# Kernel optimization log

Measured on AMD Instinct MI355X. Metric: run time of the kernel, lower is better.

Reference implementation:

```python
import jax, jax.numpy as jnp
import numpy as np

N = 100000
E = 3200000
NEG_SLOPE = 0.2


def _gat(x, W, a_src, a_dst, b, src, dst, n):
    """PyG-style GATConv (eval mode, self-loops already appended to src/dst)."""
    H, C = a_src.shape
    h = (x @ W).reshape(n, H, C)                       # [N,H,C]
    es = jnp.einsum('nhc,hc->nh', h, a_src)            # per-node src logits
    ed = jnp.einsum('nhc,hc->nh', h, a_dst)
    e = jax.nn.leaky_relu(es[src] + ed[dst], NEG_SLOPE)  # [E,H]
    m = jax.ops.segment_max(e, dst, num_segments=n)    # stable softmax per dst
    ee = jnp.exp(e - m[dst])
    z = jax.ops.segment_sum(ee, dst, num_segments=n)
    alpha = ee / z[dst]                                # softmax over in-edges
    out = jax.ops.segment_sum(h[src] * alpha[:, :, None], dst, num_segments=n)
    return out.reshape(n, H * C) + b


def setup_inputs() -> dict:
    key = jax.random.key(0)
    ks = jax.random.split(key, 25)
    rn = lambda k, s, sc=0.1: jax.random.normal(k, s, dtype=jnp.float32) * sc
    return {
        'x1': rn(ks[0], (N, 8), 1.0),
        'x2': rn(ks[1], (N, 10), 1.0),
        'edge_index': jax.random.randint(ks[2], (2, E), 0, N, dtype=jnp.int32),
        'num_nodes': N,
        'Wq': rn(ks[3], (8, 16)), 'bq': rn(ks[4], (16,)),
        'Wk': rn(ks[5], (10, 16)), 'bk': rn(ks[6], (16,)),
        'Wv': rn(ks[7], (18, 16)), 'bv': rn(ks[8], (16,)),
        'W1': rn(ks[9], (16, 32)), 'a1s': rn(ks[10], (8, 4)), 'a1d': rn(ks[11], (8, 4)), 'b1': rn(ks[12], (32,)),
        'W2': rn(ks[13], (32, 16)), 'a2s': rn(ks[14], (4, 4)), 'a2d': rn(ks[15], (4, 4)), 'b2': rn(ks[16], (16,)),
        'W3': rn(ks[17], (16, 8)), 'a3s': rn(ks[18], (2, 4)), 'a3d': rn(ks[19], (2, 4)), 'b3': rn(ks[20], (8,)),
        'Wl2': rn(ks[21], (8, 1)),
    }


def reference(x1, x2, edge_index, num_nodes, Wq, bq, Wk, bk, Wv, bv,
              W1, a1s, a1d, b1, W2, a2s, a2d, b2, W3, a3s, a3d, b3, Wl2):
    n = num_nodes
    q = x1 @ Wq + bq                                   # [N,16]
    k = x2 @ Wk + bk                                   # [N,16]
    v = jnp.concatenate([x1, x2], axis=1) @ Wv + bv    # [N,16]
    score = jnp.sum(q * k, axis=1)                     # bmm(q[:,None,:], k[:,:,None]).squeeze()
    attw = jax.nn.softmax(score)[:, None]              # softmax over all nodes
    fused = attw * v                                   # [N,16]

    sl = jnp.arange(n, dtype=edge_index.dtype)         # GATConv adds self-loops
    src = jnp.concatenate([edge_index[0], sl])
    dst = jnp.concatenate([edge_index[1], sl])

    h1 = _gat(fused, W1, a1s, a1d, b1, src, dst, n)    # [N,32]
    h2 = _gat(h1, W2, a2s, a2d, b2, src, dst, n)       # [N,16]
    x4 = _gat(h2, W3, a3s, a3d, b3, src, dst, n)       # [N,8]; dropout=identity (eval)

    # Row-normalized adjacency (no self loops), expressed as O(E) segment ops.
    r, c = edge_index[0], edge_index[1]
    deg = jax.ops.segment_sum(jnp.ones_like(r, dtype=x4.dtype), r, num_segments=n)
    inv = jnp.where(deg > 0, 1.0 / deg, 0.0)[:, None]
    R3 = jax.ops.segment_sum(x4[c], r, num_segments=n) * inv  # Adj_norm @ x4
    local = jnp.sum(x4 * R3, axis=1, keepdims=True)    # sum_j Adjn[i,j]*(x4_i . x4_j)
    glob = R3 @ Wl2                                    # lin2 (no bias)
    return local + glob                                # [N,1]
```

## Files before the change

kernel.cpp:

```cpp
#include <hip/hip_runtime.h>

#define TPB 256
#define NBMAX 1024
#define CAP 9216
#define EPB 2048

typedef float f32x4 __attribute__((ext_vector_type(4)));
typedef float f32x2 __attribute__((ext_vector_type(2)));

__device__ __forceinline__ float lrelu(float x) { return x > 0.f ? x : 0.2f * x; }

__device__ __forceinline__ unsigned bfr(float x) {
  unsigned u = __float_as_uint(x);
  return (u + 0x7FFFu + ((u >> 16) & 1u)) >> 16;
}
__device__ __forceinline__ unsigned pk(float a, float b) { return bfr(a) | (bfr(b) << 16); }
__device__ __forceinline__ float ubf(unsigned us) { return __uint_as_float(us << 16); }

__global__ void __launch_bounds__(TPB) k_bucket(
    const int* __restrict__ ei, int E, int N,
    int* __restrict__ cursor, unsigned* __restrict__ items)
{
  __shared__ int hist[NBMAX];
  __shared__ int lofs[NBMAX];
  __shared__ int basem[NBMAX];
  __shared__ int scan_s[TPB];
  __shared__ unsigned stage[2 * EPB];
  __shared__ unsigned short bid[2 * EPB];
  int tid = threadIdx.x;
  for (int i = tid; i < NBMAX; i += TPB) hist[i] = 0;
  int s0 = blockIdx.x * EPB;
  int nE = min(EPB, E - s0);
  int sv[EPB / TPB], dv[EPB / TPB];
  __syncthreads();
#pragma unroll
  for (int k = 0; k < EPB / (TPB * 4); k++) {
    int li = tid * 4 + k * TPB * 4;
    if (li + 3 < nE) {
      int4 s4 = *(const int4*)(ei + s0 + li);
      int4 d4 = *(const int4*)(ei + E + s0 + li);
      sv[k*4+0] = s4.x; sv[k*4+1] = s4.y; sv[k*4+2] = s4.z; sv[k*4+3] = s4.w;
      dv[k*4+0] = d4.x; dv[k*4+1] = d4.y; dv[k*4+2] = d4.z; dv[k*4+3] = d4.w;
#pragma unroll
      for (int j = 0; j < 4; j++) {
        atomicAdd(&hist[dv[k*4+j] >> 8], 1);
        atomicAdd(&hist[(N + sv[k*4+j]) >> 8], 1);
      }
    } else {
      for (int j = 0; j < 4; j++) {
        if (li + j < nE) {
          sv[k*4+j] = ei[s0 + li + j];
          dv[k*4+j] = ei[E + s0 + li + j];
          atomicAdd(&hist[dv[k*4+j] >> 8], 1);
          atomicAdd(&hist[(N + sv[k*4+j]) >> 8], 1);
        }
      }
    }
  }
  __syncthreads();
  int b0 = tid * 4;
  int c0 = hist[b0], c1 = hist[b0 + 1], c2 = hist[b0 + 2], c3 = hist[b0 + 3];
  int tsum = c0 + c1 + c2 + c3;
  scan_s[tid] = tsum;
  __syncthreads();
#pragma unroll
  for (int o = 1; o < TPB; o <<= 1) {
    int t = (tid >= o) ? scan_s[tid - o] : 0;
    __syncthreads();
    scan_s[tid] += t;
    __syncthreads();
  }
  int run = scan_s[tid] - tsum;
  int cs[4] = {c0, c1, c2, c3};
#pragma unroll
  for (int j = 0; j < 4; j++) {
    int b = b0 + j, c = cs[j];
    lofs[b] = run;
    int resv = c ? atomicAdd(&cursor[b], c) : 0;
    basem[b] = b * CAP + resv - run;
    hist[b] = 0;
    run += c;
  }
  __syncthreads();
#pragma unroll
  for (int k = 0; k < EPB / TPB; k++) {
    int li = tid * 4 + (k >> 2) * TPB * 4 + (k & 3);
    if (li < nE) {
      int s = sv[k], d = dv[k];
      int b1 = d >> 8;
      int p1 = lofs[b1] + atomicAdd(&hist[b1], 1);
      stage[p1] = ((unsigned)(d & 255) << 24) | (unsigned)s;
      bid[p1] = (unsigned short)b1;
      int k2 = N + s, b2 = k2 >> 8;
      int p2 = lofs[b2] + atomicAdd(&hist[b2], 1);
      stage[p2] = ((unsigned)(k2 & 255) << 24) | (unsigned)d;
      bid[p2] = (unsigned short)b2;
    }
  }
  __syncthreads();
  int total = 2 * nE;
  for (int idx = tid; idx < total; idx += TPB) {
    unsigned u = stage[idx];
    int b = bid[idx];
    int dest = basem[b] + idx;
    if (dest < (b + 1) * CAP) items[dest] = u;
  }
}

__global__ void __launch_bounds__(TPB) k_csr(
    const int* __restrict__ cursor, unsigned* __restrict__ items,
    int* __restrict__ rowptr, int* __restrict__ rowend, int n2)
{
  __shared__ unsigned stage[CAP];
  __shared__ int cnt_s[TPB], scan_s[TPB], off_s[TPB];
  int tid = threadIdx.x, b = blockIdx.x;
  size_t bbase = (size_t)b * CAP;
  int cnt = min(cursor[b], CAP);
  int c4 = cnt & ~3;
  for (int i = tid * 4; i < c4; i += TPB * 4) {
    uint4 v = *(const uint4*)(items + bbase + i);
    stage[i] = v.x; stage[i+1] = v.y; stage[i+2] = v.z; stage[i+3] = v.w;
  }
  for (int i = c4 + tid; i < cnt; i += TPB) stage[i] = items[bbase + i];
  cnt_s[tid] = 0;
  __syncthreads();
  for (int i = tid; i < cnt; i += TPB) atomicAdd(&cnt_s[stage[i] >> 24], 1);
  __syncthreads();
  int v = cnt_s[tid];
  scan_s[tid] = v;
  __syncthreads();
#pragma unroll
  for (int o = 1; o < TPB; o <<= 1) {
    int t = (tid >= o) ? scan_s[tid - o] : 0;
    __syncthreads();
    scan_s[tid] += t;
    __syncthreads();
  }
  int excl = scan_s[tid] - v;
  off_s[tid] = excl;
  int g = b * 256 + tid;
  if (g < n2) { rowptr[g] = (int)bbase + excl; rowend[g] = (int)bbase + excl + v; }
  cnt_s[tid] = 0;
  __syncthreads();
  for (int i = tid; i < cnt; i += TPB) {
    unsigned u = stage[i];
    int k = u >> 24;
    int r = atomicAdd(&cnt_s[k], 1);
    items[bbase + off_s[k] + r] = u & 0xFFFFFFu;
  }
}


__global__ void __launch_bounds__(TPB) k_score(
    const float* __restrict__ x1, const float* __restrict__ x2,
    const float* __restrict__ Wq, const float* __restrict__ bq,
    const float* __restrict__ Wk, const float* __restrict__ bk,
    float* __restrict__ escore, float* __restrict__ sumexp, int N)
{
  __shared__ float sWq[128], sWk[160], sbq[16], sbk[16];
  for (int i = threadIdx.x; i < 128; i += TPB) sWq[i] = Wq[i];
  for (int i = threadIdx.x; i < 160; i += TPB) sWk[i] = Wk[i];
  if (threadIdx.x < 16) { sbq[threadIdx.x] = bq[threadIdx.x]; sbk[threadIdx.x] = bk[threadIdx.x]; }
  __syncthreads();
  int n = blockIdx.x * TPB + threadIdx.x;
  float e = 0.f;
  if (n < N) {
    float a[8], b[10];
#pragma unroll
    for (int i = 0; i < 8; i++) a[i] = x1[n*8 + i];
#pragma unroll
    for (int i = 0; i < 10; i++) b[i] = x2[n*10 + i];
    float score = 0.f;
#pragma unroll
    for (int j = 0; j < 16; j++) {
      float q = sbq[j], k = sbk[j];
#pragma unroll
      for (int i = 0; i < 8; i++) q += a[i] * sWq[i*16 + j];
#pragma unroll
      for (int i = 0; i < 10; i++) k += b[i] * sWk[i*16 + j];
      score += q * k;
    }
    e = __expf(score);
    escore[n] = e;
  }
  float v = e;
#pragma unroll
  for (int off = 32; off > 0; off >>= 1) v += __shfl_down(v, off);
  __shared__ float red[TPB / 64];
  if ((threadIdx.x & 63) == 0) red[threadIdx.x >> 6] = v;
  __syncthreads();
  if (threadIdx.x == 0) {
    float s = 0.f;
#pragma unroll
    for (int w = 0; w < TPB / 64; w++) s += red[w];
    atomicAdd(sumexp, s);
  }
}

__global__ void __launch_bounds__(TPB) k_A1(
    const float* __restrict__ x1, const float* __restrict__ x2,
    const float* __restrict__ Wv, const float* __restrict__ bv,
    const float* __restrict__ W1, const float* __restrict__ a1s, const float* __restrict__ a1d,
    const float* __restrict__ escore, const float* __restrict__ sumexp,
    unsigned* __restrict__ rec1a, unsigned* __restrict__ rec1b,
    float* __restrict__ ed, int N)
{
  __shared__ float sWv[288], sbv[16], sW1[512], sas[32], sad[32];
  for (int i = threadIdx.x; i < 288; i += TPB) sWv[i] = Wv[i];
  for (int i = threadIdx.x; i < 512; i += TPB) sW1[i] = W1[i];
  if (threadIdx.x < 16) sbv[threadIdx.x] = bv[threadIdx.x];
  if (threadIdx.x < 32) { sas[threadIdx.x] = a1s[threadIdx.x]; sad[threadIdx.x] = a1d[threadIdx.x]; }
  __syncthreads();
  int n = blockIdx.x * TPB + threadIdx.x;
  if (n >= N) return;
  float w = escore[n] / sumexp[0];
  float f[16];
  {
    float a[8], b[10];
#pragma unroll
    for (int i = 0; i < 8; i++) a[i] = x1[n*8 + i];
#pragma unroll
    for (int i = 0; i < 10; i++) b[i] = x2[n*10 + i];
#pragma unroll
    for (int j = 0; j < 16; j++) {
      float v = sbv[j];
#pragma unroll
      for (int i = 0; i < 8; i++) v += a[i] * sWv[i*16 + j];
#pragma unroll
      for (int i = 0; i < 10; i++) v += b[i] * sWv[(8 + i)*16 + j];
      f[j] = w * v;
    }
  }
  float hr[32], esv[8], edv[8];
#pragma unroll
  for (int j = 0; j < 32; j++) {
    float s = 0.f;
#pragma unroll
    for (int i = 0; i < 16; i++) s += f[i] * sW1[i*32 + j];
    hr[j] = s;
  }
#pragma unroll
  for (int hh = 0; hh < 8; hh++) {
    float s = 0.f, d = 0.f;
#pragma unroll
    for (int c = 0; c < 4; c++) { s += hr[hh*4+c]*sas[hh*4+c]; d += hr[hh*4+c]*sad[hh*4+c]; }
    esv[hh] = s; edv[hh] = d;
  }
  unsigned* ra = rec1a + (size_t)n*10;
  unsigned* rb = rec1b + (size_t)n*10;
  ra[0] = pk(esv[0], esv[1]); ra[1] = pk(esv[2], esv[3]);
  rb[0] = pk(esv[4], esv[5]); rb[1] = pk(esv[6], esv[7]);
#pragma unroll
  for (int hh = 0; hh < 4; hh++) {
    ra[2+2*hh] = pk(hr[hh*4+0], hr[hh*4+1]);
    ra[3+2*hh] = pk(hr[hh*4+2], hr[hh*4+3]);
    rb[2+2*hh] = pk(hr[16+hh*4+0], hr[16+hh*4+1]);
    rb[3+2*hh] = pk(hr[16+hh*4+2], hr[16+hh*4+3]);
  }
  f32x4 e0 = {edv[0], edv[1], edv[2], edv[3]};
  f32x4 e1 = {edv[4], edv[5], edv[6], edv[7]};
  *(f32x4*)(ed + n*8)     = e0;
  *(f32x4*)(ed + n*8 + 4) = e1;
}

__global__ void __launch_bounds__(TPB) k_B2(
    const float* __restrict__ W2, const float* __restrict__ a2s, const float* __restrict__ a2d,
    const float* __restrict__ X,
    unsigned* __restrict__ rec2, float* __restrict__ ed, int N)
{
  __shared__ float sW[512], sas[16], sad[16];
  for (int i = threadIdx.x; i < 512; i += TPB) sW[i] = W2[i];
  if (threadIdx.x < 16) { sas[threadIdx.x] = a2s[threadIdx.x]; sad[threadIdx.x] = a2d[threadIdx.x]; }
  __syncthreads();
  int n = blockIdx.x * TPB + threadIdx.x;
  if (n >= N) return;
  float Xr[32];
#pragma unroll
  for (int i = 0; i < 8; i++) {
    f32x4 t = __builtin_nontemporal_load((const f32x4*)(X + n*32) + i);
    Xr[i*4+0] = t.x; Xr[i*4+1] = t.y; Xr[i*4+2] = t.z; Xr[i*4+3] = t.w;
  }
  float hr[16];
#pragma unroll
  for (int j = 0; j < 16; j++) {
    float s = 0.f;
#pragma unroll
    for (int f = 0; f < 32; f++) s += Xr[f] * sW[f*16 + j];
    hr[j] = s;
  }
  float esv[4], edv[4];
#pragma unroll
  for (int hh = 0; hh < 4; hh++) {
    float s = 0.f, d = 0.f;
#pragma unroll
    for (int c = 0; c < 4; c++) { s += hr[hh*4+c]*sas[hh*4+c]; d += hr[hh*4+c]*sad[hh*4+c]; }
    esv[hh] = s; edv[hh] = d;
  }
  unsigned* r = rec2 + (size_t)n*10;
  r[0] = pk(esv[0], esv[1]); r[1] = pk(esv[2], esv[3]);
#pragma unroll
  for (int hh = 0; hh < 4; hh++) {
    r[2+2*hh] = pk(hr[hh*4+0], hr[hh*4+1]);
    r[3+2*hh] = pk(hr[hh*4+2], hr[hh*4+3]);
  }
  f32x4 e0 = {edv[0], edv[1], edv[2], edv[3]};
  *(f32x4*)(ed + n*8) = e0;
}

__global__ void __launch_bounds__(TPB) k_B3(
    const float* __restrict__ W3, const float* __restrict__ a3s, const float* __restrict__ a3d,
    const float* __restrict__ X3,
    float* __restrict__ rec3, float* __restrict__ ed, int N)
{
  __shared__ float sW[128], sas[8], sad[8];
  for (int i = threadIdx.x; i < 128; i += TPB) sW[i] = W3[i];
  if (threadIdx.x < 8) { sas[threadIdx.x] = a3s[threadIdx.x]; sad[threadIdx.x] = a3d[threadIdx.x]; }
  __syncthreads();
  int n = blockIdx.x * TPB + threadIdx.x;
  if (n >= N) return;
  float Xr[16];
#pragma unroll
  for (int i = 0; i < 4; i++) {
    f32x4 t = __builtin_nontemporal_load((const f32x4*)(X3 + n*16) + i);
    Xr[i*4+0] = t.x; Xr[i*4+1] = t.y; Xr[i*4+2] = t.z; Xr[i*4+3] = t.w;
  }
  float hr[8];
#pragma unroll
  for (int j = 0; j < 8; j++) {
    float s = 0.f;
#pragma unroll
    for (int f = 0; f < 16; f++) s += Xr[f] * sW[f*8 + j];
    hr[j] = s;
  }
  float* r = rec3 + (size_t)n*10;
#pragma unroll
  for (int hh = 0; hh < 2; hh++) {
    float s = 0.f, d = 0.f;
#pragma unroll
    for (int c = 0; c < 4; c++) { s += hr[hh*4+c]*sas[hh*4+c]; d += hr[hh*4+c]*sad[hh*4+c]; }
    r[hh] = s;
    ed[n*8 + hh] = d;
  }
#pragma unroll
  for (int hh = 0; hh < 2; hh++) {
    f32x2 a = {hr[hh*4+0], hr[hh*4+1]};
    f32x2 b = {hr[hh*4+2], hr[hh*4+3]};
    *(f32x2*)(r + 2 + hh*4)     = a;
    *(f32x2*)(r + 2 + hh*4 + 2) = b;
  }
}

template<int OS, int HOFF>
__global__ void __launch_bounds__(TPB) k_gat4(
    const int* __restrict__ rowptr, const int* __restrict__ rowend, const int* __restrict__ col,
    const unsigned* __restrict__ rec, const float* __restrict__ ed,
    const float* __restrict__ bias, float* __restrict__ out, int N)
{
  int wave = (blockIdx.x * TPB + threadIdx.x) >> 6;
  if (wave >= N) return;
  int lane = threadIdx.x & 63;
  int hh = lane & 3, j = lane >> 2;
  int d = wave;
  int e0 = rowptr[d], deg = rowend[d] - e0;
  float edv = ed[d*8 + HOFF + hh];
  float z = 0.f;
  f32x4 acc = {0.f, 0.f, 0.f, 0.f};
  for (int t = j; t <= deg; t += 16) {
    int s = (t == deg) ? d : __builtin_nontemporal_load(col + e0 + t);
    const unsigned* rp = rec + (size_t)s*10;
    unsigned ew = rp[hh >> 1];
    uint2 hv = *(const uint2*)(rp + 2 + 2*hh);
    float esv = ubf((ew >> ((hh & 1) * 16)) & 0xFFFFu);
    float w = __expf(lrelu(esv + edv));
    z += w;
    acc.x += w * ubf(hv.x & 0xFFFFu); acc.y += w * ubf(hv.x >> 16);
    acc.z += w * ubf(hv.y & 0xFFFFu); acc.w += w * ubf(hv.y >> 16);
  }
#pragma unroll
  for (int m = 4; m < 64; m <<= 1) {
    z += __shfl_xor(z, m);
    acc.x += __shfl_xor(acc.x, m); acc.y += __shfl_xor(acc.y, m);
    acc.z += __shfl_xor(acc.z, m); acc.w += __shfl_xor(acc.w, m);
  }
  if (j == 0) {
    float inv = 1.f / z;
    const f32x4 bb = *(const f32x4*)(bias + (HOFF + hh)*4);
    f32x4 o = { acc.x*inv + bb.x, acc.y*inv + bb.y, acc.z*inv + bb.z, acc.w*inv + bb.w };
    __builtin_nontemporal_store(o, (f32x4*)(out + (size_t)d*OS + (HOFF + hh)*4));
  }
}

__global__ void __launch_bounds__(TPB) k_gat3(
    const int* __restrict__ rowptr, const int* __restrict__ rowend, const int* __restrict__ col,
    const float* __restrict__ rec, const float* __restrict__ ed,
    const float* __restrict__ b3, float* __restrict__ x4, int N)
{
  int wave = (blockIdx.x * TPB + threadIdx.x) >> 6;
  if (wave >= N) return;
  int lane = threadIdx.x & 63;
  int hh = lane & 1, j = lane >> 1;
  int d = wave;
  int e0 = rowptr[d], deg = rowend[d] - e0;
  float edv = ed[d*8 + hh];
  float z = 0.f;
  f32x4 acc = {0.f, 0.f, 0.f, 0.f};
  for (int t = j; t <= deg; t += 32) {
    int s = (t == deg) ? d : __builtin_nontemporal_load(col + e0 + t);
    const float* rp = rec + (size_t)s*10;
    float esv = rp[hh];
    f32x2 a = *(const f32x2*)(rp + 2 + hh*4);
    f32x2 b = *(const f32x2*)(rp + 2 + hh*4 + 2);
    float w = __expf(lrelu(esv + edv));
    z += w; acc.x += w*a.x; acc.y += w*a.y; acc.z += w*b.x; acc.w += w*b.y;
  }
#pragma unroll
  for (int m = 2; m < 64; m <<= 1) {
    z += __shfl_xor(z, m);
    acc.x += __shfl_xor(acc.x, m); acc.y += __shfl_xor(acc.y, m);
    acc.z += __shfl_xor(acc.z, m); acc.w += __shfl_xor(acc.w, m);
  }
  if (j == 0) {
    float inv = 1.f / z;
    const f32x4 bb = *(const f32x4*)(b3 + hh*4);
    f32x4 o = { acc.x*inv + bb.x, acc.y*inv + bb.y, acc.z*inv + bb.z, acc.w*inv + bb.w };
    __builtin_nontemporal_store(o, (f32x4*)(x4 + d*8 + hh*4));
  }
}

__global__ void __launch_bounds__(TPB) k_adj_final(
    const int* __restrict__ rowptr, const int* __restrict__ rowend, const int* __restrict__ col,
    const float* __restrict__ x4, const float* __restrict__ Wl2,
    float* __restrict__ out, int N)
{
  __shared__ float sW[8];
  if (threadIdx.x < 8) sW[threadIdx.x] = Wl2[threadIdx.x];
  __syncthreads();
  int wave = (blockIdx.x * TPB + threadIdx.x) >> 6;
  if (wave >= N) return;
  int lane = threadIdx.x & 63;
  int q = lane & 1, j = lane >> 1;
  int r = wave;
  int e0 = rowptr[N + r], deg = rowend[N + r] - e0;
  f32x4 acc = {0.f, 0.f, 0.f, 0.f};
  for (int t = j; t < deg; t += 32) {
    int c = __builtin_nontemporal_load(col + e0 + t);
    f32x4 xv = *(const f32x4*)(x4 + c*8 + q*4);
    acc.x += xv.x; acc.y += xv.y; acc.z += xv.z; acc.w += xv.w;
  }
#pragma unroll
  for (int m = 2; m < 64; m <<= 1) {
    acc.x += __shfl_xor(acc.x, m); acc.y += __shfl_xor(acc.y, m);
    acc.z += __shfl_xor(acc.z, m); acc.w += __shfl_xor(acc.w, m);
  }
  float part = 0.f;
  if (j == 0) {
    float inv = deg > 0 ? 1.f / (float)deg : 0.f;
    f32x4 R = { acc.x*inv, acc.y*inv, acc.z*inv, acc.w*inv };
    f32x4 xo = *(const f32x4*)(x4 + r*8 + q*4);
    part = xo.x*R.x + xo.y*R.y + xo.z*R.z + xo.w*R.w
         + R.x*sW[q*4+0] + R.y*sW[q*4+1] + R.z*sW[q*4+2] + R.w*sW[q*4+3];
  }
  part += __shfl_xor(part, 1);
  if (lane == 0) out[r] = part;
}

extern "C" void kernel_launch(void* const* d_in, const int* in_sizes, int n_in,
                              void* d_out, int out_size, void* d_ws, size_t ws_size,
                              hipStream_t stream)
{
  const float* x1  = (const float*)d_in[0];
  const float* x2  = (const float*)d_in[1];
  const int*   ei  = (const int*)d_in[2];
  const float* Wq  = (const float*)d_in[4];
  const float* bq  = (const float*)d_in[5];
  const float* Wk  = (const float*)d_in[6];
  const float* bk  = (const float*)d_in[7];
  const float* Wv  = (const float*)d_in[8];
  const float* bv  = (const float*)d_in[9];
  const float* W1  = (const float*)d_in[10];
  const float* a1s = (const float*)d_in[11];
  const float* a1d = (const float*)d_in[12];
  const float* b1  = (const float*)d_in[13];
  const float* W2  = (const float*)d_in[14];
  const float* a2s = (const float*)d_in[15];
  const float* a2d = (const float*)d_in[16];
  const float* b2  = (const float*)d_in[17];
  const float* W3  = (const float*)d_in[18];
  const float* a3s = (const float*)d_in[19];
  const float* a3d = (const float*)d_in[20];
  const float* b3  = (const float*)d_in[21];
  const float* Wl2 = (const float*)d_in[22];

  int N = in_sizes[0] / 8;
  int E = in_sizes[2] / 2;
  int n2 = 2 * N;
  int NB = (n2 + 255) >> 8;

  int* cursor   = (int*)d_ws;
  float* sumexp = (float*)(cursor + 1024);
  int* rowptr   = (int*)(sumexp + 16);
  int* rowend   = rowptr + (size_t)n2;
  unsigned* items = (unsigned*)(rowend + (size_t)n2);
  unsigned* rec1a = items + (size_t)NB * CAP;
  unsigned* rec1b = rec1a + 10ull*N;
  unsigned* rec2  = rec1b + 10ull*N;
  float* rec3     = (float*)(rec2 + 10ull*N);
  float* ed       = rec3 + 10ull*N;
  float* escore   = ed + 8ull*N;
  float* X        = escore + (size_t)N;
  float* X3 = X;
  float* x4 = (float*)rec1b;

  int gN  = (N + TPB - 1) / TPB;
  int gB  = (E + EPB - 1) / EPB;
  int g64 = (int)(((long long)N * 64 + TPB - 1) / TPB);

  (void)hipMemsetAsync(d_ws, 0, (1024 + 16) * sizeof(int), stream);

  k_bucket<<<gB, TPB, 0, stream>>>(ei, E, N, cursor, items);
  k_csr<<<NB, TPB, 0, stream>>>(cursor, items, rowptr, rowend, n2);
  int* colv = (int*)items;

  k_score<<<gN, TPB, 0, stream>>>(x1, x2, Wq, bq, Wk, bk, escore, sumexp, N);
  k_A1<<<gN, TPB, 0, stream>>>(x1, x2, Wv, bv, W1, a1s, a1d, escore, sumexp, rec1a, rec1b, ed, N);

  k_gat4<32, 0><<<g64, TPB, 0, stream>>>(rowptr, rowend, colv, rec1a, ed, b1, X, N);
  k_gat4<32, 4><<<g64, TPB, 0, stream>>>(rowptr, rowend, colv, rec1b, ed, b1, X, N);
  k_B2<<<gN, TPB, 0, stream>>>(W2, a2s, a2d, X, rec2, ed, N);
  k_gat4<16, 0><<<g64, TPB, 0, stream>>>(rowptr, rowend, colv, rec2, ed, b2, X3, N);
  k_B3<<<gN, TPB, 0, stream>>>(W3, a3s, a3d, X3, rec3, ed, N);
  k_gat3<<<g64, TPB, 0, stream>>>(rowptr, rowend, colv, rec3, ed, b3, x4, N);

  k_adj_final<<<g64, TPB, 0, stream>>>(rowptr, rowend, colv, x4, Wl2, (float*)d_out, N);
}
```

Before: 561.7 us.

## Drop CSR build and aggregate GAT edges per bucket with LDS atomics

Removes the CSR construction kernel and consumes the unsorted per-256-row buckets directly. Each block scatters edge contributions into shared-memory accumulators with atomics, in place of one wave per destination row reading a sorted column list. The source-side bucketing is padded so that each block maps to a whole set of 256 rows. This saves a full pass and the row pointer arrays. In exchange it adds many shared-memory float atomics per edge, and the summation order becomes nondeterministic.

```diff
diff --git a/kernel.cpp b/kernel.cpp
--- a/kernel.cpp
+++ b/kernel.cpp
@@ -18,7 +18,7 @@
 __device__ __forceinline__ float ubf(unsigned us) { return __uint_as_float(us << 16); }
 
 __global__ void __launch_bounds__(TPB) k_bucket(
-    const int* __restrict__ ei, int E, int N,
+    const int* __restrict__ ei, int E, int NPAD,
     int* __restrict__ cursor, unsigned* __restrict__ items)
 {
   __shared__ int hist[NBMAX];
@@ -44,7 +44,7 @@
 #pragma unroll
       for (int j = 0; j < 4; j++) {
         atomicAdd(&hist[dv[k*4+j] >> 8], 1);
-        atomicAdd(&hist[(N + sv[k*4+j]) >> 8], 1);
+        atomicAdd(&hist[(NPAD + sv[k*4+j]) >> 8], 1);
       }
     } else {
       for (int j = 0; j < 4; j++) {
@@ -52,7 +52,7 @@
           sv[k*4+j] = ei[s0 + li + j];
           dv[k*4+j] = ei[E + s0 + li + j];
           atomicAdd(&hist[dv[k*4+j] >> 8], 1);
-          atomicAdd(&hist[(N + sv[k*4+j]) >> 8], 1);
+          atomicAdd(&hist[(NPAD + sv[k*4+j]) >> 8], 1);
         }
       }
     }
@@ -91,9 +91,9 @@
       int p1 = lofs[b1] + atomicAdd(&hist[b1], 1);
       stage[p1] = ((unsigned)(d & 255) << 24) | (unsigned)s;
       bid[p1] = (unsigned short)b1;
-      int k2 = N + s, b2 = k2 >> 8;
+      int k2 = NPAD + s, b2 = k2 >> 8;
       int p2 = lofs[b2] + atomicAdd(&hist[b2], 1);
-      stage[p2] = ((unsigned)(k2 & 255) << 24) | (unsigned)d;
+      stage[p2] = ((unsigned)(s & 255) << 24) | (unsigned)d;
       bid[p2] = (unsigned short)b2;
     }
   }
@@ -104,49 +104,6 @@
     int b = bid[idx];
     int dest = basem[b] + idx;
     if (dest < (b + 1) * CAP) items[dest] = u;
-  }
-}
-
-__global__ void __launch_bounds__(TPB) k_csr(
-    const int* __restrict__ cursor, unsigned* __restrict__ items,
-    int* __restrict__ rowptr, int* __restrict__ rowend, int n2)
-{
-  __shared__ unsigned stage[CAP];
-  __shared__ int cnt_s[TPB], scan_s[TPB], off_s[TPB];
-  int tid = threadIdx.x, b = blockIdx.x;
-  size_t bbase = (size_t)b * CAP;
-  int cnt = min(cursor[b], CAP);
-  int c4 = cnt & ~3;
-  for (int i = tid * 4; i < c4; i += TPB * 4) {
-    uint4 v = *(const uint4*)(items + bbase + i);
-    stage[i] = v.x; stage[i+1] = v.y; stage[i+2] = v.z; stage[i+3] = v.w;
-  }
-  for (int i = c4 + tid; i < cnt; i += TPB) stage[i] = items[bbase + i];
-  cnt_s[tid] = 0;
-  __syncthreads();
-  for (int i = tid; i < cnt; i += TPB) atomicAdd(&cnt_s[stage[i] >> 24], 1);
-  __syncthreads();
-  int v = cnt_s[tid];
-  scan_s[tid] = v;
-  __syncthreads();
-#pragma unroll
-  for (int o = 1; o < TPB; o <<= 1) {
-    int t = (tid >= o) ? scan_s[tid - o] : 0;
-    __syncthreads();
-    scan_s[tid] += t;
-    __syncthreads();
-  }
-  int excl = scan_s[tid] - v;
-  off_s[tid] = excl;
-  int g = b * 256 + tid;
-  if (g < n2) { rowptr[g] = (int)bbase + excl; rowend[g] = (int)bbase + excl + v; }
-  cnt_s[tid] = 0;
-  __syncthreads();
-  for (int i = tid; i < cnt; i += TPB) {
-    unsigned u = stage[i];
-    int k = u >> 24;
-    int r = atomicAdd(&cnt_s[k], 1);
-    items[bbase + off_s[k] + r] = u & 0xFFFFFFu;
   }
 }
 
@@ -351,117 +308,178 @@
 }
 
 template<int OS, int HOFF>
-__global__ void __launch_bounds__(TPB) k_gat4(
-    const int* __restrict__ rowptr, const int* __restrict__ rowend, const int* __restrict__ col,
+__global__ void __launch_bounds__(TPB) k_gatb(
+    const int* __restrict__ cursor, const unsigned* __restrict__ items,
     const unsigned* __restrict__ rec, const float* __restrict__ ed,
     const float* __restrict__ bias, float* __restrict__ out, int N)
 {
-  int wave = (blockIdx.x * TPB + threadIdx.x) >> 6;
-  if (wave >= N) return;
-  int lane = threadIdx.x & 63;
-  int hh = lane & 3, j = lane >> 2;
-  int d = wave;
-  int e0 = rowptr[d], deg = rowend[d] - e0;
-  float edv = ed[d*8 + HOFF + hh];
-  float z = 0.f;
-  f32x4 acc = {0.f, 0.f, 0.f, 0.f};
-  for (int t = j; t <= deg; t += 16) {
-    int s = (t == deg) ? d : __builtin_nontemporal_load(col + e0 + t);
+  __shared__ float zacc[256][21];
+  __shared__ float eds[256][4];
+  int tid = threadIdx.x, b = blockIdx.x;
+  int base = b << 8;
+  {
+    int r = base + tid;
+    f32x4 e = {0.f, 0.f, 0.f, 0.f};
+    if (r < N) e = *(const f32x4*)(ed + (size_t)r*8 + HOFF);
+    eds[tid][0] = e.x; eds[tid][1] = e.y; eds[tid][2] = e.z; eds[tid][3] = e.w;
+#pragma unroll
+    for (int i = 0; i < 21; i++) zacc[tid][i] = 0.f;
+  }
+  __syncthreads();
+  size_t bbase = (size_t)b * CAP;
+  int cnt = min(cursor[b], CAP);
+  for (int i = tid; i < cnt; i += TPB) {
+    unsigned u = __builtin_nontemporal_load(items + bbase + i);
+    int row = u >> 24;
+    int s = u & 0xFFFFFFu;
     const unsigned* rp = rec + (size_t)s*10;
-    unsigned ew = rp[hh >> 1];
-    uint2 hv = *(const uint2*)(rp + 2 + 2*hh);
-    float esv = ubf((ew >> ((hh & 1) * 16)) & 0xFFFFu);
-    float w = __expf(lrelu(esv + edv));
-    z += w;
-    acc.x += w * ubf(hv.x & 0xFFFFu); acc.y += w * ubf(hv.x >> 16);
-    acc.z += w * ubf(hv.y & 0xFFFFu); acc.w += w * ubf(hv.y >> 16);
-  }
-#pragma unroll
-  for (int m = 4; m < 64; m <<= 1) {
-    z += __shfl_xor(z, m);
-    acc.x += __shfl_xor(acc.x, m); acc.y += __shfl_xor(acc.y, m);
-    acc.z += __shfl_xor(acc.z, m); acc.w += __shfl_xor(acc.w, m);
-  }
-  if (j == 0) {
+    uint2 ew  = *(const uint2*)rp;
+    uint4 h01 = *(const uint4*)(rp + 2);
+    uint4 h23 = *(const uint4*)(rp + 6);
+    unsigned hw[8] = {h01.x, h01.y, h01.z, h01.w, h23.x, h23.y, h23.z, h23.w};
+    float esv[4] = {ubf(ew.x & 0xFFFFu), ubf(ew.x >> 16),
+                    ubf(ew.y & 0xFFFFu), ubf(ew.y >> 16)};
+    float* za = &zacc[row][0];
+#pragma unroll
+    for (int hh = 0; hh < 4; hh++) {
+      float w = __expf(lrelu(esv[hh] + eds[row][hh]));
+      atomicAdd(&za[hh*5 + 0], w);
+      unsigned a = hw[2*hh], c = hw[2*hh + 1];
+      atomicAdd(&za[hh*5 + 1], w * ubf(a & 0xFFFFu));
+      atomicAdd(&za[hh*5 + 2], w * ubf(a >> 16));
+      atomicAdd(&za[hh*5 + 3], w * ubf(c & 0xFFFFu));
+      atomicAdd(&za[hh*5 + 4], w * ubf(c >> 16));
+    }
+  }
+  __syncthreads();
+  int r = base + tid;
+  if (r >= N) return;
+  const unsigned* rp = rec + (size_t)r*10;
+  uint2 ew  = *(const uint2*)rp;
+  uint4 h01 = *(const uint4*)(rp + 2);
+  uint4 h23 = *(const uint4*)(rp + 6);
+  unsigned hw[8] = {h01.x, h01.y, h01.z, h01.w, h23.x, h23.y, h23.z, h23.w};
+  float esv[4] = {ubf(ew.x & 0xFFFFu), ubf(ew.x >> 16),
+                  ubf(ew.y & 0xFFFFu), ubf(ew.y >> 16)};
+#pragma unroll
+  for (int hh = 0; hh < 4; hh++) {
+    float w = __expf(lrelu(esv[hh] + eds[tid][hh]));
+    float z = zacc[tid][hh*5 + 0] + w;
+    unsigned a = hw[2*hh], c = hw[2*hh + 1];
     float inv = 1.f / z;
     const f32x4 bb = *(const f32x4*)(bias + (HOFF + hh)*4);
-    f32x4 o = { acc.x*inv + bb.x, acc.y*inv + bb.y, acc.z*inv + bb.z, acc.w*inv + bb.w };
-    __builtin_nontemporal_store(o, (f32x4*)(out + (size_t)d*OS + (HOFF + hh)*4));
-  }
-}
-
-__global__ void __launch_bounds__(TPB) k_gat3(
-    const int* __restrict__ rowptr, const int* __restrict__ rowend, const int* __restrict__ col,
+    f32x4 o = { (zacc[tid][hh*5+1] + w*ubf(a & 0xFFFFu))*inv + bb.x,
+                (zacc[tid][hh*5+2] + w*ubf(a >> 16))   *inv + bb.y,
+                (zacc[tid][hh*5+3] + w*ubf(c & 0xFFFFu))*inv + bb.z,
+                (zacc[tid][hh*5+4] + w*ubf(c >> 16))   *inv + bb.w };
+    __builtin_nontemporal_store(o, (f32x4*)(out + (size_t)r*OS + (HOFF + hh)*4));
+  }
+}
+
+__global__ void __launch_bounds__(TPB) k_gat3b(
+    const int* __restrict__ cursor, const unsigned* __restrict__ items,
     const float* __restrict__ rec, const float* __restrict__ ed,
     const float* __restrict__ b3, float* __restrict__ x4, int N)
 {
-  int wave = (blockIdx.x * TPB + threadIdx.x) >> 6;
-  if (wave >= N) return;
-  int lane = threadIdx.x & 63;
-  int hh = lane & 1, j = lane >> 1;
-  int d = wave;
-  int e0 = rowptr[d], deg = rowend[d] - e0;
-  float edv = ed[d*8 + hh];
-  float z = 0.f;
-  f32x4 acc = {0.f, 0.f, 0.f, 0.f};
-  for (int t = j; t <= deg; t += 32) {
-    int s = (t == deg) ? d : __builtin_nontemporal_load(col + e0 + t);
+  __shared__ float zacc[256][11];
+  __shared__ float eds[256][2];
+  int tid = threadIdx.x, b = blockIdx.x;
+  int base = b << 8;
+  {
+    int r = base + tid;
+    f32x2 e = {0.f, 0.f};
+    if (r < N) e = *(const f32x2*)(ed + (size_t)r*8);
+    eds[tid][0] = e.x; eds[tid][1] = e.y;
+#pragma unroll
+    for (int i = 0; i < 11; i++) zacc[tid][i] = 0.f;
+  }
+  __syncthreads();
+  size_t bbase = (size_t)b * CAP;
+  int cnt = min(cursor[b], CAP);
+  for (int i = tid; i < cnt; i += TPB) {
+    unsigned u = __builtin_nontemporal_load(items + bbase + i);
+    int row = u >> 24;
+    int s = u & 0xFFFFFFu;
     const float* rp = rec + (size_t)s*10;
-    float esv = rp[hh];
-    f32x2 a = *(const f32x2*)(rp + 2 + hh*4);
-    f32x2 b = *(const f32x2*)(rp + 2 + hh*4 + 2);
-    float w = __expf(lrelu(esv + edv));
-    z += w; acc.x += w*a.x; acc.y += w*a.y; acc.z += w*b.x; acc.w += w*b.y;
-  }
-#pragma unroll
-  for (int m = 2; m < 64; m <<= 1) {
-    z += __shfl_xor(z, m);
-    acc.x += __shfl_xor(acc.x, m); acc.y += __shfl_xor(acc.y, m);
-    acc.z += __shfl_xor(acc.z, m); acc.w += __shfl_xor(acc.w, m);
-  }
-  if (j == 0) {
-    float inv = 1.f / z;
-    const f32x4 bb = *(const f32x4*)(b3 + hh*4);
-    f32x4 o = { acc.x*inv + bb.x, acc.y*inv + bb.y, acc.z*inv + bb.z, acc.w*inv + bb.w };
-    __builtin_nontemporal_store(o, (f32x4*)(x4 + d*8 + hh*4));
-  }
-}
-
-__global__ void __launch_bounds__(TPB) k_adj_final(
-    const int* __restrict__ rowptr, const int* __restrict__ rowend, const int* __restrict__ col,
+    f32x2 es2 = *(const f32x2*)rp;
+    f32x4 h0 = *(const f32x4*)(rp + 2);
+    f32x4 h1 = *(const f32x4*)(rp + 6);
+    float* za = &zacc[row][0];
+    float w0 = __expf(lrelu(es2.x + eds[row][0]));
+    atomicAdd(&za[0], w0);
+    atomicAdd(&za[1], w0*h0.x); atomicAdd(&za[2], w0*h0.y);
+    atomicAdd(&za[3], w0*h0.z); atomicAdd(&za[4], w0*h0.w);
+    float w1 = __expf(lrelu(es2.y + eds[row][1]));
+    atomicAdd(&za[5], w1);
+    atomicAdd(&za[6], w1*h1.x); atomicAdd(&za[7], w1*h1.y);
+    atomicAdd(&za[8], w1*h1.z); atomicAdd(&za[9], w1*h1.w);
+  }
+  __syncthreads();
+  int r = base + tid;
+  if (r >= N) return;
+  const float* rp = rec + (size_t)r*10;
+  f32x2 es2 = *(const f32x2*)rp;
+  f32x4 h0 = *(const f32x4*)(rp + 2);
+  f32x4 h1 = *(const f32x4*)(rp + 6);
+  float w0 = __expf(lrelu(es2.x + eds[tid][0]));
+  float w1 = __expf(lrelu(es2.y + eds[tid][1]));
+  float i0 = 1.f / (zacc[tid][0] + w0);
+  float i1 = 1.f / (zacc[tid][5] + w1);
+  const f32x4 bb0 = *(const f32x4*)(b3);
+  const f32x4 bb1 = *(const f32x4*)(b3 + 4);
+  f32x4 o0 = { (zacc[tid][1] + w0*h0.x)*i0 + bb0.x, (zacc[tid][2] + w0*h0.y)*i0 + bb0.y,
+               (zacc[tid][3] + w0*h0.z)*i0 + bb0.z, (zacc[tid][4] + w0*h0.w)*i0 + bb0.w };
+  f32x4 o1 = { (zacc[tid][6] + w1*h1.x)*i1 + bb1.x, (zacc[tid][7] + w1*h1.y)*i1 + bb1.y,
+               (zacc[tid][8] + w1*h1.z)*i1 + bb1.z, (zacc[tid][9] + w1*h1.w)*i1 + bb1.w };
+  __builtin_nontemporal_store(o0, (f32x4*)(x4 + (size_t)r*8));
+  __builtin_nontemporal_store(o1, (f32x4*)(x4 + (size_t)r*8 + 4));
+}
+
+__global__ void __launch_bounds__(TPB) k_adjb(
+    const int* __restrict__ cursor, const unsigned* __restrict__ items,
     const float* __restrict__ x4, const float* __restrict__ Wl2,
-    float* __restrict__ out, int N)
-{
+    float* __restrict__ out, int N, int NBD)
+{
+  __shared__ float racc[256][9];
   __shared__ float sW[8];
-  if (threadIdx.x < 8) sW[threadIdx.x] = Wl2[threadIdx.x];
-  __syncthreads();
-  int wave = (blockIdx.x * TPB + threadIdx.x) >> 6;
-  if (wave >= N) return;
-  int lane = threadIdx.x & 63;
-  int q = lane & 1, j = lane >> 1;
-  int r = wave;
-  int e0 = rowptr[N + r], deg = rowend[N + r] - e0;
-  f32x4 acc = {0.f, 0.f, 0.f, 0.f};
-  for (int t = j; t < deg; t += 32) {
-    int c = __builtin_nontemporal_load(col + e0 + t);
-    f32x4 xv = *(const f32x4*)(x4 + c*8 + q*4);
-    acc.x += xv.x; acc.y += xv.y; acc.z += xv.z; acc.w += xv.w;
-  }
-#pragma unroll
-  for (int m = 2; m < 64; m <<= 1) {
-    acc.x += __shfl_xor(acc.x, m); acc.y += __shfl_xor(acc.y, m);
-    acc.z += __shfl_xor(acc.z, m); acc.w += __shfl_xor(acc.w, m);
-  }
-  float part = 0.f;
-  if (j == 0) {
-    float inv = deg > 0 ? 1.f / (float)deg : 0.f;
-    f32x4 R = { acc.x*inv, acc.y*inv, acc.z*inv, acc.w*inv };
-    f32x4 xo = *(const f32x4*)(x4 + r*8 + q*4);
-    part = xo.x*R.x + xo.y*R.y + xo.z*R.z + xo.w*R.w
-         + R.x*sW[q*4+0] + R.y*sW[q*4+1] + R.z*sW[q*4+2] + R.w*sW[q*4+3];
-  }
-  part += __shfl_xor(part, 1);
-  if (lane == 0) out[r] = part;
+  int tid = threadIdx.x, b = blockIdx.x + NBD;
+  int base = blockIdx.x << 8;
+  if (tid < 8) sW[tid] = Wl2[tid];
+#pragma unroll
+  for (int i = 0; i < 9; i++) racc[tid][i] = 0.f;
+  __syncthreads();
+  size_t bbase = (size_t)b * CAP;
+  int cnt = min(cursor[b], CAP);
+  for (int i = tid; i < cnt; i += TPB) {
+    unsigned u = __builtin_nontemporal_load(items + bbase + i);
+    int row = u >> 24;
+    int c = u & 0xFFFFFFu;
+    f32x4 xv0 = *(const f32x4*)(x4 + (size_t)c*8);
+    f32x4 xv1 = *(const f32x4*)(x4 + (size_t)c*8 + 4);
+    float* ra = &racc[row][0];
+    atomicAdd(&ra[0], xv0.x); atomicAdd(&ra[1], xv0.y);
+    atomicAdd(&ra[2], xv0.z); atomicAdd(&ra[3], xv0.w);
+    atomicAdd(&ra[4], xv1.x); atomicAdd(&ra[5], xv1.y);
+    atomicAdd(&ra[6], xv1.z); atomicAdd(&ra[7], xv1.w);
+    atomicAdd(&ra[8], 1.f);
+  }
+  __syncthreads();
+  int r = base + tid;
+  if (r >= N) return;
+  float deg = racc[tid][8];
+  float inv = deg > 0.f ? 1.f / deg : 0.f;
+  f32x4 xo0 = *(const f32x4*)(x4 + (size_t)r*8);
+  f32x4 xo1 = *(const f32x4*)(x4 + (size_t)r*8 + 4);
+  float res = 0.f;
+#pragma unroll
+  for (int j = 0; j < 4; j++) {
+    float R0 = racc[tid][j] * inv;
+    float R1 = racc[tid][4 + j] * inv;
+    float x0 = (j==0)?xo0.x:(j==1)?xo0.y:(j==2)?xo0.z:xo0.w;
+    float x1 = (j==0)?xo1.x:(j==1)?xo1.y:(j==2)?xo1.z:xo1.w;
+    res += R0 * (x0 + sW[j]) + R1 * (x1 + sW[4 + j]);
+  }
+  out[r] = res;
 }
 
 extern "C" void kernel_launch(void* const* d_in, const int* in_sizes, int n_in,
@@ -493,14 +511,13 @@
 
   int N = in_sizes[0] / 8;
   int E = in_sizes[2] / 2;
-  int n2 = 2 * N;
-  int NB = (n2 + 255) >> 8;
+  int NBD  = (N + 255) >> 8;
+  int NPAD = NBD << 8;
+  int NB   = NBD + NBD;
 
   int* cursor   = (int*)d_ws;
   float* sumexp = (float*)(cursor + 1024);
-  int* rowptr   = (int*)(sumexp + 16);
-  int* rowend   = rowptr + (size_t)n2;
-  unsigned* items = (unsigned*)(rowend + (size_t)n2);
+  unsigned* items = (unsigned*)(sumexp + 16);
   unsigned* rec1a = items + (size_t)NB * CAP;
   unsigned* rec1b = rec1a + 10ull*N;
   unsigned* rec2  = rec1b + 10ull*N;
@@ -513,23 +530,20 @@
 
   int gN  = (N + TPB - 1) / TPB;
   int gB  = (E + EPB - 1) / EPB;
-  int g64 = (int)(((long long)N * 64 + TPB - 1) / TPB);
 
   (void)hipMemsetAsync(d_ws, 0, (1024 + 16) * sizeof(int), stream);
 
-  k_bucket<<<gB, TPB, 0, stream>>>(ei, E, N, cursor, items);
-  k_csr<<<NB, TPB, 0, stream>>>(cursor, items, rowptr, rowend, n2);
-  int* colv = (int*)items;
+  k_bucket<<<gB, TPB, 0, stream>>>(ei, E, NPAD, cursor, items);
 
   k_score<<<gN, TPB, 0, stream>>>(x1, x2, Wq, bq, Wk, bk, escore, sumexp, N);
   k_A1<<<gN, TPB, 0, stream>>>(x1, x2, Wv, bv, W1, a1s, a1d, escore, sumexp, rec1a, rec1b, ed, N);
 
-  k_gat4<32, 0><<<g64, TPB, 0, stream>>>(rowptr, rowend, colv, rec1a, ed, b1, X, N);
-  k_gat4<32, 4><<<g64, TPB, 0, stream>>>(rowptr, rowend, colv, rec1b, ed, b1, X, N);
+  k_gatb<32, 0><<<NBD, TPB, 0, stream>>>(cursor, items, rec1a, ed, b1, X, N);
+  k_gatb<32, 4><<<NBD, TPB, 0, stream>>>(cursor, items, rec1b, ed, b1, X, N);
   k_B2<<<gN, TPB, 0, stream>>>(W2, a2s, a2d, X, rec2, ed, N);
-  k_gat4<16, 0><<<g64, TPB, 0, stream>>>(rowptr, rowend, colv, rec2, ed, b2, X3, N);
+  k_gatb<16, 0><<<NBD, TPB, 0, stream>>>(cursor, items, rec2, ed, b2, X3, N);
   k_B3<<<gN, TPB, 0, stream>>>(W3, a3s, a3d, X3, rec3, ed, N);
-  k_gat3<<<g64, TPB, 0, stream>>>(rowptr, rowend, colv, rec3, ed, b3, x4, N);
-
-  k_adj_final<<<g64, TPB, 0, stream>>>(rowptr, rowend, colv, x4, Wl2, (float*)d_out, N);
-}
+  k_gat3b<<<NBD, TPB, 0, stream>>>(cursor, items, rec3, ed, b3, x4, N);
+
+  k_adjb<<<NBD, TPB, 0, stream>>>(cursor, items, x4, Wl2, (float*)d_out, N, NBD);
+}
```

Measured after the change: 1.970 ms. +250.7%, slower.

## Replace atomic bucket cursors with per-block segment offsets and gather-based CSR build

Applied to the files above, without the earlier changes.

The bucketing kernel no longer reserves space in global buckets with atomics. Each block now writes its locally sorted edge records contiguously and exports its per-bucket prefix offsets. The CSR kernel then gathers each bucket's segments from every block, using the offset table to compute destinations. This removes the global atomic cursors, the bid array and the scattered writes. It also doubles edges per block, but the gather loop reads short per-block segments serially per thread, which may be poorly coalesced.

```diff
diff --git a/kernel.cpp b/kernel.cpp
--- a/kernel.cpp
+++ b/kernel.cpp
@@ -1,9 +1,9 @@
 #include <hip/hip_runtime.h>
 
 #define TPB 256
-#define NBMAX 1024
 #define CAP 9216
-#define EPB 2048
+#define EPB 4096
+#define OFSW 784
 
 typedef float f32x4 __attribute__((ext_vector_type(4)));
 typedef float f32x2 __attribute__((ext_vector_type(2)));
@@ -19,22 +19,20 @@
 
 __global__ void __launch_bounds__(TPB) k_bucket(
     const int* __restrict__ ei, int E, int N,
-    int* __restrict__ cursor, unsigned* __restrict__ items)
-{
-  __shared__ int hist[NBMAX];
-  __shared__ int lofs[NBMAX];
-  __shared__ int basem[NBMAX];
+    unsigned* __restrict__ items2, int* __restrict__ ofs)
+{
+  __shared__ int hist[1024];
+  __shared__ int lofs[1024];
   __shared__ int scan_s[TPB];
   __shared__ unsigned stage[2 * EPB];
-  __shared__ unsigned short bid[2 * EPB];
   int tid = threadIdx.x;
-  for (int i = tid; i < NBMAX; i += TPB) hist[i] = 0;
+  for (int i = tid; i < 1024; i += TPB) hist[i] = 0;
   int s0 = blockIdx.x * EPB;
   int nE = min(EPB, E - s0);
-  int sv[EPB / TPB], dv[EPB / TPB];
-  __syncthreads();
-#pragma unroll
-  for (int k = 0; k < EPB / (TPB * 4); k++) {
+  int sv[16], dv[16];
+  __syncthreads();
+#pragma unroll
+  for (int k = 0; k < 4; k++) {
     int li = tid * 4 + k * TPB * 4;
     if (li + 3 < nE) {
       int4 s4 = *(const int4*)(ei + s0 + li);
@@ -74,55 +72,65 @@
   int cs[4] = {c0, c1, c2, c3};
 #pragma unroll
   for (int j = 0; j < 4; j++) {
-    int b = b0 + j, c = cs[j];
+    int b = b0 + j;
     lofs[b] = run;
-    int resv = c ? atomicAdd(&cursor[b], c) : 0;
-    basem[b] = b * CAP + resv - run;
     hist[b] = 0;
-    run += c;
-  }
-  __syncthreads();
-#pragma unroll
-  for (int k = 0; k < EPB / TPB; k++) {
+    run += cs[j];
+  }
+  __syncthreads();
+#pragma unroll
+  for (int k = 0; k < 16; k++) {
     int li = tid * 4 + (k >> 2) * TPB * 4 + (k & 3);
     if (li < nE) {
       int s = sv[k], d = dv[k];
       int b1 = d >> 8;
       int p1 = lofs[b1] + atomicAdd(&hist[b1], 1);
       stage[p1] = ((unsigned)(d & 255) << 24) | (unsigned)s;
-      bid[p1] = (unsigned short)b1;
       int k2 = N + s, b2 = k2 >> 8;
       int p2 = lofs[b2] + atomicAdd(&hist[b2], 1);
       stage[p2] = ((unsigned)(k2 & 255) << 24) | (unsigned)d;
-      bid[p2] = (unsigned short)b2;
     }
   }
   __syncthreads();
   int total = 2 * nE;
-  for (int idx = tid; idx < total; idx += TPB) {
-    unsigned u = stage[idx];
-    int b = bid[idx];
-    int dest = basem[b] + idx;
-    if (dest < (b + 1) * CAP) items[dest] = u;
-  }
-}
-
-__global__ void __launch_bounds__(TPB) k_csr(
-    const int* __restrict__ cursor, unsigned* __restrict__ items,
-    int* __restrict__ rowptr, int* __restrict__ rowend, int n2)
+  size_t obase = (size_t)blockIdx.x * (2 * EPB);
+  for (int idx = tid; idx < total; idx += TPB)
+    __builtin_nontemporal_store(stage[idx], items2 + obase + idx);
+  int orow = blockIdx.x * OFSW;
+  for (int i = tid; i < OFSW; i += TPB)
+    ofs[orow + i] = lofs[i];
+}
+
+__global__ void __launch_bounds__(TPB) k_csr2(
+    const int* __restrict__ ofs, const unsigned* __restrict__ items2, int nB,
+    unsigned* __restrict__ items, int* __restrict__ rowptr, int* __restrict__ rowend, int n2)
 {
   __shared__ unsigned stage[CAP];
+  __shared__ int segdst[OFSW];
+  __shared__ int ctr;
   __shared__ int cnt_s[TPB], scan_s[TPB], off_s[TPB];
-  int tid = threadIdx.x, b = blockIdx.x;
-  size_t bbase = (size_t)b * CAP;
-  int cnt = min(cursor[b], CAP);
-  int c4 = cnt & ~3;
-  for (int i = tid * 4; i < c4; i += TPB * 4) {
-    uint4 v = *(const uint4*)(items + bbase + i);
-    stage[i] = v.x; stage[i+1] = v.y; stage[i+2] = v.z; stage[i+3] = v.w;
-  }
-  for (int i = c4 + tid; i < cnt; i += TPB) stage[i] = items[bbase + i];
+  int tid = threadIdx.x, k = blockIdx.x;
+  if (tid == 0) ctr = 0;
   cnt_s[tid] = 0;
+  __syncthreads();
+  for (int b = tid; b < nB; b += TPB) {
+    int o0 = ofs[b * OFSW + k];
+    int o1 = ofs[b * OFSW + k + 1];
+    int c = o1 - o0;
+    segdst[b] = c ? atomicAdd(&ctr, c) : 0;
+  }
+  __syncthreads();
+  int cnt = min(ctr, CAP);
+  for (int b = tid; b < nB; b += TPB) {
+    int o0 = ofs[b * OFSW + k];
+    int c  = ofs[b * OFSW + k + 1] - o0;
+    int dst = segdst[b];
+    const unsigned* src = items2 + (size_t)b * (2 * EPB) + o0;
+    for (int j = 0; j < c; j++) {
+      int p = dst + j;
+      if (p < CAP) stage[p] = __builtin_nontemporal_load(src + j);
+    }
+  }
   __syncthreads();
   for (int i = tid; i < cnt; i += TPB) atomicAdd(&cnt_s[stage[i] >> 24], 1);
   __syncthreads();
@@ -138,15 +146,16 @@
   }
   int excl = scan_s[tid] - v;
   off_s[tid] = excl;
-  int g = b * 256 + tid;
+  size_t bbase = (size_t)k * CAP;
+  int g = k * 256 + tid;
   if (g < n2) { rowptr[g] = (int)bbase + excl; rowend[g] = (int)bbase + excl + v; }
   cnt_s[tid] = 0;
   __syncthreads();
   for (int i = tid; i < cnt; i += TPB) {
     unsigned u = stage[i];
-    int k = u >> 24;
-    int r = atomicAdd(&cnt_s[k], 1);
-    items[bbase + off_s[k] + r] = u & 0xFFFFFFu;
+    int kk = u >> 24;
+    int r = atomicAdd(&cnt_s[kk], 1);
+    items[bbase + off_s[kk] + r] = u & 0xFFFFFFu;
   }
 }
 
@@ -495,31 +504,34 @@
   int E = in_sizes[2] / 2;
   int n2 = 2 * N;
   int NB = (n2 + 255) >> 8;
-
-  int* cursor   = (int*)d_ws;
-  float* sumexp = (float*)(cursor + 1024);
+  int gB = (E + EPB - 1) / EPB;
+
+  float* sumexp = (float*)d_ws;
   int* rowptr   = (int*)(sumexp + 16);
   int* rowend   = rowptr + (size_t)n2;
-  unsigned* items = (unsigned*)(rowend + (size_t)n2);
-  unsigned* rec1a = items + (size_t)NB * CAP;
+  unsigned* itemsCSR = (unsigned*)(rowend + (size_t)n2);
+  unsigned* regionA  = itemsCSR + (size_t)NB * CAP;
+  unsigned* items2 = regionA;
+  int* ofs = (int*)(items2 + (size_t)gB * (2 * EPB));
+  size_t raSize = (size_t)gB * (2 * EPB + OFSW);
+  unsigned* rec1a = regionA;
   unsigned* rec1b = rec1a + 10ull*N;
   unsigned* rec2  = rec1b + 10ull*N;
   float* rec3     = (float*)(rec2 + 10ull*N);
   float* ed       = rec3 + 10ull*N;
   float* escore   = ed + 8ull*N;
-  float* X        = escore + (size_t)N;
+  float* X        = (float*)(regionA + raSize);
   float* X3 = X;
   float* x4 = (float*)rec1b;
 
-  int gN  = (N + TPB - 1) / TPB;
-  int gB  = (E + EPB - 1) / EPB;
+  int gN = (N + TPB - 1) / TPB;
   int g64 = (int)(((long long)N * 64 + TPB - 1) / TPB);
 
-  (void)hipMemsetAsync(d_ws, 0, (1024 + 16) * sizeof(int), stream);
-
-  k_bucket<<<gB, TPB, 0, stream>>>(ei, E, N, cursor, items);
-  k_csr<<<NB, TPB, 0, stream>>>(cursor, items, rowptr, rowend, n2);
-  int* colv = (int*)items;
+  (void)hipMemsetAsync(sumexp, 0, 16 * sizeof(float), stream);
+
+  k_bucket<<<gB, TPB, 0, stream>>>(ei, E, N, items2, ofs);
+  k_csr2<<<NB, TPB, 0, stream>>>(ofs, items2, gB, itemsCSR, rowptr, rowend, n2);
+  int* colv = (int*)itemsCSR;
 
   k_score<<<gN, TPB, 0, stream>>>(x1, x2, Wq, bq, Wk, bk, escore, sumexp, N);
   k_A1<<<gN, TPB, 0, stream>>>(x1, x2, Wv, bv, W1, a1s, a1d, escore, sumexp, rec1a, rec1b, ed, N);
```

New measurement: 582.3 us. 3.7% more time.
